# Kernel optimization log

Measured on AMD Instinct MI355X. Metric: run time of the kernel, lower is better.

The kernel has to match this reference:

```python
import jax, jax.numpy as jnp
import numpy as np

B, D, H, L = 8, 512, 512, 8192


def _log_g(x):
    # log_g(x) = log(relu(x)+1) if x>=0 else x
    return jnp.where(x >= 0, jnp.log1p(jax.nn.relu(x)), x)


def setup_inputs() -> dict:
    key = jax.random.key(0)
    k1, k2, k3 = jax.random.split(key, 3)
    x = jax.random.normal(k1, (B, D, L), dtype=jnp.float32)
    # Conv1d(dim, 2*h_dim, kernel_size=1) weight [2H, D, 1] squeezed to [2H, D]
    W = jax.random.normal(k2, (2 * H, D), dtype=jnp.float32) / np.sqrt(D).astype(np.float32)
    b = jax.random.normal(k3, (2 * H,), dtype=jnp.float32) * 0.02
    return {"x": x, "W": W, "b": b}


def reference(x, W, b):
    # 1x1 conv == pointwise linear over channels: [B, 2H, L]
    hg = jnp.einsum('od,bdl->bol', W, x) + b[None, :, None]
    h, gate = jnp.split(hg, 2, axis=1)  # each [B, H, L]
    log_coeffs = -jax.nn.softplus(gate)                 # log(1 - sigmoid(gate))
    log_values = -jax.nn.softplus(-gate) + _log_g(h)    # log(sigmoid(gate)) + log_g(h)
    a_star = jnp.cumsum(log_coeffs, axis=2)
    log_h = a_star + jax.lax.cumlogsumexp(log_values - a_star, axis=2)
    return jnp.exp(log_h)  # [B, H, L]
```

## Files before the change

### kernel.cpp

```cpp
#include <hip/hip_runtime.h>
#include <hip/hip_fp16.h>

#define B_  8
#define D_  512
#define H_  512
#define L_  8192
#define O2_ 1024

typedef __attribute__((ext_vector_type(8))) short   bf16x8;
typedef __attribute__((ext_vector_type(4))) float   floatx4;
typedef __attribute__((ext_vector_type(8))) unsigned short ushort8_t;
typedef __attribute__((ext_vector_type(4))) unsigned short ushort4_t;

__device__ __forceinline__ unsigned short f2bf(float f) {
    union { float f; unsigned u; } x; x.f = f;
    unsigned u = x.u;
    u += 0x7FFFu + ((u >> 16) & 1u);
    return (unsigned short)(u >> 16);
}

__device__ __forceinline__ void async_load16(const void* g, void* l) {
    __builtin_amdgcn_global_load_lds(
        (const __attribute__((address_space(1))) unsigned int*)g,
        (__attribute__((address_space(3))) unsigned int*)l,
        16, 0, 0);
}

__global__ __launch_bounds__(256) void prep_w(const float* __restrict__ W,
                                              unsigned short* __restrict__ Wr) {
    int idx  = blockIdx.x * 256 + threadIdx.x;
    int flat = idx * 4;
    int o = flat >> 9;
    int d = flat & 511;
    int src_o = (o & 1) ? (H_ + (o >> 1)) : (o >> 1);
    float4 wv = *(const float4*)(W + (size_t)src_o * D_ + d);
    ushort4_t r;
    r.x = f2bf(wv.x); r.y = f2bf(wv.y); r.z = f2bf(wv.z); r.w = f2bf(wv.w);
    *(ushort4_t*)(Wr + (size_t)o * D_ + d) = r;
}

__global__ __launch_bounds__(256) void transpose_x(const float* __restrict__ x,
                                                   unsigned short* __restrict__ xT) {
    __shared__ float T[64][65];
    const int b  = blockIdx.z;
    const int d0 = blockIdx.y * 64;
    const int l0 = blockIdx.x * 64;
    const int tid = threadIdx.x;

    const int c  = tid & 15;
    const int r0 = tid >> 4;
    const float* xp = x + ((size_t)b * D_ + d0) * L_ + l0;
    for (int rr = r0; rr < 64; rr += 16) {
        float4 vv = *(const float4*)(xp + (size_t)rr * L_ + c * 4);
        T[c * 4 + 0][rr] = vv.x;
        T[c * 4 + 1][rr] = vv.y;
        T[c * 4 + 2][rr] = vv.z;
        T[c * 4 + 3][rr] = vv.w;
    }
    __syncthreads();

    const int dc  = (tid & 7) * 8;
    const int lr0 = tid >> 3;
    unsigned short* op = xT + ((size_t)b * L_ + l0) * D_ + d0;
    for (int lr = lr0; lr < 64; lr += 32) {
        ushort8_t o8;
        o8[0] = f2bf(T[lr][dc + 0]); o8[1] = f2bf(T[lr][dc + 1]);
        o8[2] = f2bf(T[lr][dc + 2]); o8[3] = f2bf(T[lr][dc + 3]);
        o8[4] = f2bf(T[lr][dc + 4]); o8[5] = f2bf(T[lr][dc + 5]);
        o8[6] = f2bf(T[lr][dc + 6]); o8[7] = f2bf(T[lr][dc + 7]);
        *(ushort8_t*)(op + (size_t)lr * D_ + dc) = o8;
    }
}

__global__ __launch_bounds__(256) void gemm_hg(const unsigned short* __restrict__ Wr,
                                               const unsigned short* __restrict__ xT,
                                               __half* __restrict__ hg) {
    __shared__ __align__(16) unsigned short As[128][64];
    __shared__ __align__(16) unsigned short Bs[128][64];

    const int b  = blockIdx.z;
    const int o0 = blockIdx.y * 128;
    const int l0 = blockIdx.x * 128;
    const int tid  = threadIdx.x;
    const int lane = tid & 63;
    const int w    = tid >> 6;
    const int wm   = (w >> 1) * 64;
    const int wn   = (w & 1) * 64;
    const int lm   = lane & 15;
    const int quad = lane >> 4;

    floatx4 acc[4][4];
    for (int mi = 0; mi < 4; ++mi)
        for (int ni = 0; ni < 4; ++ni)
            acc[mi][ni] = (floatx4){0.f, 0.f, 0.f, 0.f};

    const int sj  = lane >> 3;
    const int scg = (lane & 7) ^ sj;
    const unsigned short* Ag = Wr + (size_t)(o0 + w * 32 + sj) * D_ + scg * 8;
    const unsigned short* Bg = xT + ((size_t)b * L_ + l0 + w * 32 + sj) * D_ + scg * 8;

    for (int kk = 0; kk < 8; ++kk) {
        const int k0 = kk * 64;
        #pragma unroll
        for (int p = 0; p < 4; ++p) {
            async_load16(Ag + (size_t)(p * 8) * D_ + k0, &As[w * 32 + p * 8][0]);
            async_load16(Bg + (size_t)(p * 8) * D_ + k0, &Bs[w * 32 + p * 8][0]);
        }
        __syncthreads();

        #pragma unroll
        for (int ks = 0; ks < 2; ++ks) {
            const int lc = ks * 4 + quad;
            bf16x8 af[4], bfv[4];
            #pragma unroll
            for (int mi = 0; mi < 4; ++mi) {
                const int r = wm + mi * 16 + lm;
                af[mi] = *(const bf16x8*)&As[r][(lc ^ (r & 7)) * 8];
            }
            #pragma unroll
            for (int ni = 0; ni < 4; ++ni) {
                const int r = wn + ni * 16 + lm;
                bfv[ni] = *(const bf16x8*)&Bs[r][(lc ^ (r & 7)) * 8];
            }
            #pragma unroll
            for (int mi = 0; mi < 4; ++mi)
                #pragma unroll
                for (int ni = 0; ni < 4; ++ni)
                    acc[mi][ni] = __builtin_amdgcn_mfma_f32_16x16x32_bf16(
                        af[mi], bfv[ni], acc[mi][ni], 0, 0, 0);
        }
        __syncthreads();
    }

    __half* hp = hg + ((size_t)b * O2_ + o0 + wm + quad * 4) * L_ + l0 + wn + lm;
    for (int mi = 0; mi < 4; ++mi)
        for (int ni = 0; ni < 4; ++ni)
            for (int r = 0; r < 4; ++r)
                hp[(size_t)(mi * 16 + r) * L_ + ni * 16] = __float2half(acc[mi][ni][r]);
}

__global__ __launch_bounds__(256) void scan_seq(const __half* __restrict__ hg,
                                                const float* __restrict__ bias,
                                                float* __restrict__ out) {
    __shared__ __align__(16) unsigned int sBuf[256 * 40];
    __shared__ float wA[4];
    __shared__ float wB[4];
    unsigned int* sH = sBuf;
    unsigned int* sG = sBuf + 256 * 20;

    const int bid = blockIdx.x;
    const int b = bid >> 9;
    const int k = bid & 511;
    const int t = threadIdx.x;
    const int lane = t & 63;
    const int wid  = t >> 6;

    const uint4* hq = (const uint4*)(hg + ((size_t)b * O2_ + 2 * k) * L_);
    const uint4* gq = hq + (L_ / 8);

    #pragma unroll
    for (int j = 0; j < 4; ++j) {
        int idx = t + 256 * j;
        uint4 hv = hq[idx];
        uint4 gv = gq[idx];
        int cc = idx >> 2, ss = idx & 3;
        *(uint4*)&sH[cc * 20 + ss * 4] = hv;
        *(uint4*)&sG[cc * 20 + ss * 4] = gv;
    }
    const float bh = bias[k];
    const float bg = bias[H_ + k];
    __syncthreads();

    float c[32], v[32];
    float A = 1.f, Bv = 0.f;
    #pragma unroll
    for (int j4 = 0; j4 < 4; ++j4) {
        uint4 hv = *(const uint4*)&sH[t * 20 + j4 * 4];
        uint4 gv = *(const uint4*)&sG[t * 20 + j4 * 4];
        unsigned hu[4] = {hv.x, hv.y, hv.z, hv.w};
        unsigned gu[4] = {gv.x, gv.y, gv.z, gv.w};
        #pragma unroll
        for (int q = 0; q < 4; ++q) {
            __half2 h2 = *(const __half2*)&hu[q];
            __half2 g2 = *(const __half2*)&gu[q];
            #pragma unroll
            for (int e = 0; e < 2; ++e) {
                const int i = j4 * 8 + q * 2 + e;
                float hf = (e ? __high2float(h2) : __low2float(h2)) + bh;
                float gf = (e ? __high2float(g2) : __low2float(g2)) + bg;
                float ex  = __expf(gf);
                float inv = 1.f / (1.f + ex);
                float ci  = inv;
                float zi  = ex * inv;
                float gv2 = (hf >= 0.f) ? (1.f + hf) : __expf(hf);
                float vi  = zi * gv2;
                c[i] = ci; v[i] = vi;
                Bv = ci * Bv + vi;
                A *= ci;
            }
        }
    }

    #pragma unroll
    for (int off = 1; off < 64; off <<= 1) {
        float pA = __shfl_up(A, off);
        float pB = __shfl_up(Bv, off);
        if (lane >= off) { Bv = Bv + A * pB; A = A * pA; }
    }

    if (lane == 63) { wA[wid] = A; wB[wid] = Bv; }
    __syncthreads();

    float cB = 0.f;
    for (int p = 0; p < wid; ++p) cB = wB[p] + wA[p] * cB;

    float eA = __shfl_up(A, 1);
    float eB = __shfl_up(Bv, 1);
    if (lane == 0) { eA = 1.f; eB = 0.f; }
    float hr = eB + eA * cB;

    float* sO = (float*)sBuf;
    #pragma unroll
    for (int i = 0; i < 32; i += 4) {
        float4 o4;
        o4.x = hr = c[i + 0] * hr + v[i + 0];
        o4.y = hr = c[i + 1] * hr + v[i + 1];
        o4.z = hr = c[i + 2] * hr + v[i + 2];
        o4.w = hr = c[i + 3] * hr + v[i + 3];
        *(float4*)&sO[t * 36 + i] = o4;
    }
    __syncthreads();

    float4* op4 = (float4*)(out + ((size_t)b * H_ + k) * L_);
    #pragma unroll
    for (int j = 0; j < 8; ++j) {
        int idx = t + 256 * j;
        int cc = idx >> 3, ss = idx & 7;
        op4[idx] = *(const float4*)&sO[cc * 36 + ss * 4];
    }
}

__global__ __launch_bounds__(256) void fused_naive(const float* __restrict__ x,
                                                   const float* __restrict__ W,
                                                   const float* __restrict__ bias,
                                                   float* __restrict__ out) {
    __shared__ float Wh[512];
    __shared__ float Wg[512];
    __shared__ float sA[256];
    __shared__ float sB[256];
    const int bid = blockIdx.x;
    const int b = bid >> 9;
    const int k = bid & 511;
    const int t = threadIdx.x;

    for (int i = t; i < 512; i += 256) {
        Wh[i] = W[(size_t)k * D_ + i];
        Wg[i] = W[(size_t)(H_ + k) * D_ + i];
    }
    const float bh = bias[k];
    const float bg = bias[H_ + k];
    __syncthreads();

    float Hc = 0.f;
    const float* xb = x + (size_t)b * D_ * L_;
    for (int ch = 0; ch < 32; ++ch) {
        const int l = ch * 256 + t;
        float ah = bh, ag = bg;
        for (int d = 0; d < 512; ++d) {
            float xv = xb[(size_t)d * L_ + l];
            ah += Wh[d] * xv;
            ag += Wg[d] * xv;
        }
        float e   = __expf(ag);
        float inv = 1.f / (1.f + e);
        float ci  = inv;
        float zi  = e * inv;
        float gv  = (ah >= 0.f) ? (1.f + ah) : __expf(ah);
        float vi  = zi * gv;

        float A = ci, Bv = vi;
        sA[t] = A; sB[t] = Bv;
        __syncthreads();
        for (int off = 1; off < 256; off <<= 1) {
            float pA = 1.f, pB = 0.f;
            if (t >= off) { pA = sA[t - off]; pB = sB[t - off]; }
            __syncthreads();
            Bv = Bv + A * pB;
            A  = A * pA;
            sA[t] = A; sB[t] = Bv;
            __syncthreads();
        }
        out[((size_t)b * H_ + k) * L_ + l] = A * Hc + Bv;
        float An = sA[255], Bn = sB[255];
        Hc = An * Hc + Bn;
        __syncthreads();
    }
}

extern "C" void kernel_launch(void* const* d_in, const int* in_sizes, int n_in,
                              void* d_out, int out_size, void* d_ws, size_t ws_size,
                              hipStream_t stream) {
    const float* x    = (const float*)d_in[0];
    const float* W    = (const float*)d_in[1];
    const float* bias = (const float*)d_in[2];
    float* out = (float*)d_out;

    const size_t xT_bytes = (size_t)B_ * L_ * D_ * 2;
    const size_t Wr_bytes = (size_t)O2_ * D_ * 2;
    const size_t hg_bytes = (size_t)B_ * O2_ * L_ * 2;
    const size_t need = xT_bytes + Wr_bytes + hg_bytes;

    if (ws_size >= need) {
        char* ws = (char*)d_ws;
        unsigned short* xT = (unsigned short*)ws;
        unsigned short* Wr = (unsigned short*)(ws + xT_bytes);
        __half*         hg = (__half*)(ws + xT_bytes + Wr_bytes);

        prep_w<<<512, 256, 0, stream>>>(W, Wr);
        transpose_x<<<dim3(L_ / 64, D_ / 64, B_), 256, 0, stream>>>(x, xT);
        gemm_hg<<<dim3(L_ / 128, O2_ / 128, B_), 256, 0, stream>>>(Wr, xT, hg);
        scan_seq<<<B_ * H_, 256, 0, stream>>>(hg, bias, out);
    } else {
        fused_naive<<<B_ * H_, 256, 0, stream>>>(x, W, bias, out);
    }
}
```

Before: 352.0 us.

## Replace GEMM with 256x256-tile, 512-thread kernel using 4-stage async LDS pipeline

Replaces the 128x128 single-buffered GEMM with a 256x256-tile kernel of 8 waves. It uses a 4-deep ring of 32-wide K slices in LDS filled by async global-to-LDS loads, explicit vmcnt waits, split barriers and setprio around the MFMA bursts. Loads for future K steps can then overlap with matrix math, and the larger tile reuses more data per LDS byte. In exchange it uses more registers and LDS per block (roughly 128KB), which limits occupancy, and it launches fewer blocks.

New measurement: 367.1 us. 1.04x slower.

```diff
diff --git a/kernel.cpp b/kernel.cpp
--- a/kernel.cpp
+++ b/kernel.cpp
@@ -25,6 +25,8 @@
         (__attribute__((address_space(3))) unsigned int*)l,
         16, 0, 0);
 }
+
+#define WAITVM(N) asm volatile("s_waitcnt vmcnt(" #N ")" ::: "memory")
 
 __global__ __launch_bounds__(256) void prep_w(const float* __restrict__ W,
                                               unsigned short* __restrict__ Wr) {
@@ -72,69 +74,116 @@
     }
 }
 
-__global__ __launch_bounds__(256) void gemm_hg(const unsigned short* __restrict__ Wr,
-                                               const unsigned short* __restrict__ xT,
-                                               __half* __restrict__ hg) {
-    __shared__ __align__(16) unsigned short As[128][64];
-    __shared__ __align__(16) unsigned short Bs[128][64];
+__global__ __launch_bounds__(512, 2) void gemm_hg256(const unsigned short* __restrict__ Wr,
+                                                     const unsigned short* __restrict__ xT,
+                                                     __half* __restrict__ hg) {
+    __shared__ __align__(16) unsigned short As[4 * 256 * 32];
+    __shared__ __align__(16) unsigned short Bs[4 * 256 * 32];
 
     const int b  = blockIdx.z;
-    const int o0 = blockIdx.y * 128;
-    const int l0 = blockIdx.x * 128;
+    const int o0 = blockIdx.y * 256;
+    const int l0 = blockIdx.x * 256;
     const int tid  = threadIdx.x;
     const int lane = tid & 63;
     const int w    = tid >> 6;
-    const int wm   = (w >> 1) * 64;
-    const int wn   = (w & 1) * 64;
+    const int wm   = (w >> 2) * 128;
+    const int wn   = (w & 3) * 64;
     const int lm   = lane & 15;
     const int quad = lane >> 4;
 
-    floatx4 acc[4][4];
-    for (int mi = 0; mi < 4; ++mi)
+    const int pq = (quad ^ ((lm >> 1) & 3)) * 8;
+    int offA[8], offB[4];
+    #pragma unroll
+    for (int mi = 0; mi < 8; ++mi) offA[mi] = (wm + mi * 16 + lm) * 32 + pq;
+    #pragma unroll
+    for (int ni = 0; ni < 4; ++ni) offB[ni] = (wn + ni * 16 + lm) * 32 + pq;
+
+    const int sr  = lane >> 2;
+    const int scg = (lane & 3) ^ ((lane >> 3) & 3);
+    const unsigned short* Ag0 = Wr + (size_t)(o0 + w * 16 + sr) * D_ + scg * 8;
+    const unsigned short* Bg0 = xT + ((size_t)b * L_ + l0 + w * 16 + sr) * D_ + scg * 8;
+    const int ldsP0 = w * 512;
+    const int ldsP1 = 4096 + w * 512;
+
+    floatx4 acc[8][4];
+    #pragma unroll
+    for (int mi = 0; mi < 8; ++mi)
+        #pragma unroll
         for (int ni = 0; ni < 4; ++ni)
             acc[mi][ni] = (floatx4){0.f, 0.f, 0.f, 0.f};
 
-    const int sj  = lane >> 3;
-    const int scg = (lane & 7) ^ sj;
-    const unsigned short* Ag = Wr + (size_t)(o0 + w * 32 + sj) * D_ + scg * 8;
-    const unsigned short* Bg = xT + ((size_t)b * L_ + l0 + w * 32 + sj) * D_ + scg * 8;
-
-    for (int kk = 0; kk < 8; ++kk) {
-        const int k0 = kk * 64;
+    #pragma unroll
+    for (int t = 0; t < 3; ++t) {
+        async_load16(Ag0 + (size_t)t * 32,                    &As[t * 8192 + ldsP0]);
+        async_load16(Ag0 + (size_t)t * 32 + 128 * (size_t)D_, &As[t * 8192 + ldsP1]);
+        async_load16(Bg0 + (size_t)t * 32,                    &Bs[t * 8192 + ldsP0]);
+        async_load16(Bg0 + (size_t)t * 32 + 128 * (size_t)D_, &Bs[t * 8192 + ldsP1]);
+    }
+    WAITVM(8);
+    __builtin_amdgcn_s_barrier();
+
+#define GEMM_TILE(BUF, T, DO_STAGE, VMW)                                          \
+  {                                                                               \
+    bf16x8 af[4], bfv[4];                                                         \
+    const int base_ = (BUF) * 8192;                                               \
+    _Pragma("unroll")                                                             \
+    for (int mi_ = 0; mi_ < 4; ++mi_)                                             \
+        af[mi_] = *(const bf16x8*)&As[base_ + offA[mi_]];                         \
+    _Pragma("unroll")                                                             \
+    for (int ni_ = 0; ni_ < 4; ++ni_)                                             \
+        bfv[ni_] = *(const bf16x8*)&Bs[base_ + offB[ni_]];                        \
+    if (DO_STAGE) {                                                               \
+        const int nb_ = ((T) + 3) & 3;                                            \
+        async_load16(Ag0 + (size_t)((T) + 3) * 32,                    &As[nb_ * 8192 + ldsP0]); \
+        async_load16(Ag0 + (size_t)((T) + 3) * 32 + 128 * (size_t)D_, &As[nb_ * 8192 + ldsP1]); \
+    }                                                                             \
+    __builtin_amdgcn_s_barrier();                                                 \
+    __builtin_amdgcn_s_setprio(1);                                                \
+    _Pragma("unroll")                                                             \
+    for (int mi_ = 0; mi_ < 4; ++mi_)                                             \
+        _Pragma("unroll")                                                         \
+        for (int ni_ = 0; ni_ < 4; ++ni_)                                         \
+            acc[mi_][ni_] = __builtin_amdgcn_mfma_f32_16x16x32_bf16(              \
+                af[mi_], bfv[ni_], acc[mi_][ni_], 0, 0, 0);                       \
+    __builtin_amdgcn_s_setprio(0);                                                \
+    __builtin_amdgcn_s_barrier();                                                 \
+    _Pragma("unroll")                                                             \
+    for (int mi_ = 0; mi_ < 4; ++mi_)                                             \
+        af[mi_] = *(const bf16x8*)&As[base_ + offA[4 + mi_]];                     \
+    if (DO_STAGE) {                                                               \
+        const int nb_ = ((T) + 3) & 3;                                            \
+        async_load16(Bg0 + (size_t)((T) + 3) * 32,                    &Bs[nb_ * 8192 + ldsP0]); \
+        async_load16(Bg0 + (size_t)((T) + 3) * 32 + 128 * (size_t)D_, &Bs[nb_ * 8192 + ldsP1]); \
+    }                                                                             \
+    __builtin_amdgcn_s_barrier();                                                 \
+    __builtin_amdgcn_s_setprio(1);                                                \
+    _Pragma("unroll")                                                             \
+    for (int mi_ = 0; mi_ < 4; ++mi_)                                             \
+        _Pragma("unroll")                                                         \
+        for (int ni_ = 0; ni_ < 4; ++ni_)                                         \
+            acc[4 + mi_][ni_] = __builtin_amdgcn_mfma_f32_16x16x32_bf16(          \
+                af[mi_], bfv[ni_], acc[4 + mi_][ni_], 0, 0, 0);                   \
+    __builtin_amdgcn_s_setprio(0);                                                \
+    VMW;                                                                          \
+    __builtin_amdgcn_s_barrier();                                                 \
+  }
+
+    #pragma unroll 1
+    for (int t = 0; t < 13; ++t) {
+        GEMM_TILE(t & 3, t, true, WAITVM(8));
+    }
+    GEMM_TILE(1, 13, false, WAITVM(4));
+    GEMM_TILE(2, 14, false, WAITVM(0));
+    GEMM_TILE(3, 15, false, (void)0);
+
+#undef GEMM_TILE
+
+    __half* hp = hg + ((size_t)b * O2_ + o0 + wm + quad * 4) * L_ + l0 + wn + lm;
+    #pragma unroll
+    for (int mi = 0; mi < 8; ++mi)
         #pragma unroll
-        for (int p = 0; p < 4; ++p) {
-            async_load16(Ag + (size_t)(p * 8) * D_ + k0, &As[w * 32 + p * 8][0]);
-            async_load16(Bg + (size_t)(p * 8) * D_ + k0, &Bs[w * 32 + p * 8][0]);
-        }
-        __syncthreads();
-
-        #pragma unroll
-        for (int ks = 0; ks < 2; ++ks) {
-            const int lc = ks * 4 + quad;
-            bf16x8 af[4], bfv[4];
+        for (int ni = 0; ni < 4; ++ni)
             #pragma unroll
-            for (int mi = 0; mi < 4; ++mi) {
-                const int r = wm + mi * 16 + lm;
-                af[mi] = *(const bf16x8*)&As[r][(lc ^ (r & 7)) * 8];
-            }
-            #pragma unroll
-            for (int ni = 0; ni < 4; ++ni) {
-                const int r = wn + ni * 16 + lm;
-                bfv[ni] = *(const bf16x8*)&Bs[r][(lc ^ (r & 7)) * 8];
-            }
-            #pragma unroll
-            for (int mi = 0; mi < 4; ++mi)
-                #pragma unroll
-                for (int ni = 0; ni < 4; ++ni)
-                    acc[mi][ni] = __builtin_amdgcn_mfma_f32_16x16x32_bf16(
-                        af[mi], bfv[ni], acc[mi][ni], 0, 0, 0);
-        }
-        __syncthreads();
-    }
-
-    __half* hp = hg + ((size_t)b * O2_ + o0 + wm + quad * 4) * L_ + l0 + wn + lm;
-    for (int mi = 0; mi < 4; ++mi)
-        for (int ni = 0; ni < 4; ++ni)
             for (int r = 0; r < 4; ++r)
                 hp[(size_t)(mi * 16 + r) * L_ + ni * 16] = __float2half(acc[mi][ni][r]);
 }
@@ -318,7 +367,7 @@
 
         prep_w<<<512, 256, 0, stream>>>(W, Wr);
         transpose_x<<<dim3(L_ / 64, D_ / 64, B_), 256, 0, stream>>>(x, xT);
-        gemm_hg<<<dim3(L_ / 128, O2_ / 128, B_), 256, 0, stream>>>(Wr, xT, hg);
+        gemm_hg256<<<dim3(L_ / 256, O2_ / 256, B_), 512, 0, stream>>>(Wr, xT, hg);
         scan_seq<<<B_ * H_, 256, 0, stream>>>(hg, bias, out);
     } else {
         fused_naive<<<B_ * H_, 256, 0, stream>>>(x, W, bias, out);
```

## Fuse x transpose and bf16 conversion into GEMM via register-prefetched tiles

Applied to the files above, without the earlier changes.

Removes the separate transpose_x kernel and its bf16 xT intermediate. The GEMM now loads fp32 x tiles into registers, converts them to bf16 and writes them transposed into a swizzled LDS layout. The next k-slice is prefetched into registers during the MFMA work, and the grid order is swapped so the 8 o-blocks sharing an x tile run adjacently and can reuse it through cache. This saves one global write and one read of the activations, at the cost of extra register pressure, 8x redundant fp32 loads and conversion of x across o-blocks, and a hand-written barrier sequence.

Result: slower. 405.0 us (+15.0%).

```diff
diff --git a/kernel.cpp b/kernel.cpp
--- a/kernel.cpp
+++ b/kernel.cpp
@@ -39,48 +39,15 @@
     *(ushort4_t*)(Wr + (size_t)o * D_ + d) = r;
 }
 
-__global__ __launch_bounds__(256) void transpose_x(const float* __restrict__ x,
-                                                   unsigned short* __restrict__ xT) {
-    __shared__ float T[64][65];
-    const int b  = blockIdx.z;
-    const int d0 = blockIdx.y * 64;
-    const int l0 = blockIdx.x * 64;
-    const int tid = threadIdx.x;
-
-    const int c  = tid & 15;
-    const int r0 = tid >> 4;
-    const float* xp = x + ((size_t)b * D_ + d0) * L_ + l0;
-    for (int rr = r0; rr < 64; rr += 16) {
-        float4 vv = *(const float4*)(xp + (size_t)rr * L_ + c * 4);
-        T[c * 4 + 0][rr] = vv.x;
-        T[c * 4 + 1][rr] = vv.y;
-        T[c * 4 + 2][rr] = vv.z;
-        T[c * 4 + 3][rr] = vv.w;
-    }
-    __syncthreads();
-
-    const int dc  = (tid & 7) * 8;
-    const int lr0 = tid >> 3;
-    unsigned short* op = xT + ((size_t)b * L_ + l0) * D_ + d0;
-    for (int lr = lr0; lr < 64; lr += 32) {
-        ushort8_t o8;
-        o8[0] = f2bf(T[lr][dc + 0]); o8[1] = f2bf(T[lr][dc + 1]);
-        o8[2] = f2bf(T[lr][dc + 2]); o8[3] = f2bf(T[lr][dc + 3]);
-        o8[4] = f2bf(T[lr][dc + 4]); o8[5] = f2bf(T[lr][dc + 5]);
-        o8[6] = f2bf(T[lr][dc + 6]); o8[7] = f2bf(T[lr][dc + 7]);
-        *(ushort8_t*)(op + (size_t)lr * D_ + dc) = o8;
-    }
-}
-
-__global__ __launch_bounds__(256) void gemm_hg(const unsigned short* __restrict__ Wr,
-                                               const unsigned short* __restrict__ xT,
-                                               __half* __restrict__ hg) {
+__global__ __launch_bounds__(256) void gemm_fused(const float* __restrict__ x,
+                                                  const unsigned short* __restrict__ Wr,
+                                                  __half* __restrict__ hg) {
     __shared__ __align__(16) unsigned short As[128][64];
     __shared__ __align__(16) unsigned short Bs[128][64];
 
     const int b  = blockIdx.z;
-    const int o0 = blockIdx.y * 128;
-    const int l0 = blockIdx.x * 128;
+    const int o0 = blockIdx.x * 128;
+    const int l0 = blockIdx.y * 128;
     const int tid  = threadIdx.x;
     const int lane = tid & 63;
     const int w    = tid >> 6;
@@ -89,24 +56,50 @@
     const int lm   = lane & 15;
     const int quad = lane >> 4;
 
-    floatx4 acc[4][4];
-    for (int mi = 0; mi < 4; ++mi)
-        for (int ni = 0; ni < 4; ++ni)
-            acc[mi][ni] = (floatx4){0.f, 0.f, 0.f, 0.f};
-
     const int sj  = lane >> 3;
     const int scg = (lane & 7) ^ sj;
     const unsigned short* Ag = Wr + (size_t)(o0 + w * 32 + sj) * D_ + scg * 8;
-    const unsigned short* Bg = xT + ((size_t)b * L_ + l0 + w * 32 + sj) * D_ + scg * 8;
+
+    const int c = tid & 31;
+    const int g = tid >> 5;
+    const float* xg = x + ((size_t)b * D_ + g * 8) * L_ + l0 + c * 4;
+
+    float4 xr[8];
+    #pragma unroll
+    for (int rr = 0; rr < 8; ++rr)
+        xr[rr] = *(const float4*)(xg + (size_t)rr * L_);
+
+    floatx4 acc[4][4];
+    #pragma unroll
+    for (int mi = 0; mi < 4; ++mi)
+        #pragma unroll
+        for (int ni = 0; ni < 4; ++ni)
+            acc[mi][ni] = (floatx4){0.f, 0.f, 0.f, 0.f};
 
     for (int kk = 0; kk < 8; ++kk) {
         const int k0 = kk * 64;
         #pragma unroll
-        for (int p = 0; p < 4; ++p) {
+        for (int p = 0; p < 4; ++p)
             async_load16(Ag + (size_t)(p * 8) * D_ + k0, &As[w * 32 + p * 8][0]);
-            async_load16(Bg + (size_t)(p * 8) * D_ + k0, &Bs[w * 32 + p * 8][0]);
-        }
+
+        #pragma unroll
+        for (int j = 0; j < 4; ++j) {
+            ushort8_t o8;
+            #pragma unroll
+            for (int rr = 0; rr < 8; ++rr)
+                o8[rr] = f2bf(((const float*)&xr[rr])[j]);
+            const int l    = c * 4 + j;
+            const int phys = g ^ (l & 7);
+            *(ushort8_t*)((char*)&Bs[l][0] + phys * 16) = o8;
+        }
+
         __syncthreads();
+
+        if (kk < 7) {
+            #pragma unroll
+            for (int rr = 0; rr < 8; ++rr)
+                xr[rr] = *(const float4*)(xg + (size_t)((kk + 1) * 64 + rr) * L_);
+        }
 
         #pragma unroll
         for (int ks = 0; ks < 2; ++ks) {
@@ -129,7 +122,10 @@
                     acc[mi][ni] = __builtin_amdgcn_mfma_f32_16x16x32_bf16(
                         af[mi], bfv[ni], acc[mi][ni], 0, 0, 0);
         }
-        __syncthreads();
+
+        asm volatile("s_waitcnt lgkmcnt(0)" ::: "memory");
+        __builtin_amdgcn_s_barrier();
+        asm volatile("" ::: "memory");
     }
 
     __half* hp = hg + ((size_t)b * O2_ + o0 + wm + quad * 4) * L_ + l0 + wn + lm;
@@ -305,20 +301,17 @@
     const float* bias = (const float*)d_in[2];
     float* out = (float*)d_out;
 
-    const size_t xT_bytes = (size_t)B_ * L_ * D_ * 2;
     const size_t Wr_bytes = (size_t)O2_ * D_ * 2;
     const size_t hg_bytes = (size_t)B_ * O2_ * L_ * 2;
-    const size_t need = xT_bytes + Wr_bytes + hg_bytes;
+    const size_t need = Wr_bytes + hg_bytes;
 
     if (ws_size >= need) {
         char* ws = (char*)d_ws;
-        unsigned short* xT = (unsigned short*)ws;
-        unsigned short* Wr = (unsigned short*)(ws + xT_bytes);
-        __half*         hg = (__half*)(ws + xT_bytes + Wr_bytes);
+        unsigned short* Wr = (unsigned short*)ws;
+        __half*         hg = (__half*)(ws + Wr_bytes);
 
         prep_w<<<512, 256, 0, stream>>>(W, Wr);
-        transpose_x<<<dim3(L_ / 64, D_ / 64, B_), 256, 0, stream>>>(x, xT);
-        gemm_hg<<<dim3(L_ / 128, O2_ / 128, B_), 256, 0, stream>>>(Wr, xT, hg);
+        gemm_fused<<<dim3(O2_ / 128, L_ / 128, B_), 256, 0, stream>>>(x, Wr, hg);
         scan_seq<<<B_ * H_, 256, 0, stream>>>(hg, bias, out);
     } else {
         fused_naive<<<B_ * H_, 256, 0, stream>>>(x, W, bias, out);
```
